# Kernel optimization log

Measured on AMD Instinct MI355X. Metric: run time of the kernel, lower is better.

## Reference

```python
import jax, jax.numpy as jnp
import numpy as np
import math

BATCH, SEQLEN, DMODEL, NSTATE, DFF = 4, 2048, 1024, 16, 4096
EPS = 1e-6


def rmsnorm(x, scale):
    return x * jax.lax.rsqrt(jnp.mean(x * x, axis=-1, keepdims=True) + EPS) * scale


def ssm_scan(u, A_ssm, B_ssm, C_ssm, D_ssm):
    # u: (B, L, D). Diagonal SSM per (d, n) channel/state pair.
    dt = jnp.exp(jnp.linspace(math.log(0.001), math.log(0.1), NSTATE))  # (N,)
    expA = jnp.exp(A_ssm)                 # (D, N); continuous A = -expA
    dA = jnp.exp(-expA * dt)              # (D, N) discrete decay
    dB = B_ssm * (1.0 - dA) / expA        # (D, N) ZOH input matrix

    def step(s, u_t):
        # s: (B, D, N), u_t: (B, D)
        s = s * dA + u_t[..., None] * dB
        y = jnp.einsum('bdn,dn->bd', s, C_ssm)
        return s, y

    s0 = jnp.zeros((u.shape[0], DMODEL, NSTATE), dtype=u.dtype)
    _, ys = jax.lax.scan(step, s0, jnp.transpose(u, (1, 0, 2)))  # ys: (L, B, D)
    return jnp.transpose(ys, (1, 0, 2)) + u * D_ssm


def setup_inputs() -> dict:
    key = jax.random.key(0)
    ks = jax.random.split(key, 6)
    return {
        'x': jax.random.normal(ks[0], (BATCH, SEQLEN, DMODEL), jnp.float32),
        'A_ssm': jax.random.normal(ks[1], (DMODEL, NSTATE), jnp.float32),
        'B_ssm': jax.random.normal(ks[2], (DMODEL, NSTATE), jnp.float32),
        'C_ssm': jax.random.normal(ks[3], (DMODEL, NSTATE), jnp.float32),
        'D_ssm': jnp.zeros((DMODEL,), jnp.float32),
        'scale1': jnp.ones((DMODEL,), jnp.float32),
        'scale2': jnp.ones((DMODEL,), jnp.float32),
        'w1': jax.random.normal(ks[4], (DMODEL, DFF), jnp.float32) * 0.02,
        'b1': jnp.zeros((DFF,), jnp.float32),
        'w2': jax.random.normal(ks[5], (DFF, DMODEL), jnp.float32) * 0.02,
        'b2': jnp.zeros((DMODEL,), jnp.float32),
    }


def reference(x, A_ssm, B_ssm, C_ssm, D_ssm, scale1, scale2, w1, b1, w2, b2):
    x = x + ssm_scan(rmsnorm(x, scale1), A_ssm, B_ssm, C_ssm, D_ssm)
    h = rmsnorm(x, scale2)
    h = jax.nn.gelu(h @ w1 + b1, approximate=False) @ w2 + b2
    return x + h
```

## Files before the change

kernel.cpp:

```cpp
#include <hip/hip_runtime.h>
#include <cstdint>
#include <cstddef>


#define BATCH 4
#define SEQLEN 2048
#define DMODEL 1024
#define NSTATE 16
#define DFF 4096
#define NCH 32
#define LCH 64

typedef unsigned short ushort_t;
typedef __attribute__((ext_vector_type(8))) short short8;
typedef __attribute__((ext_vector_type(4))) float f32x4;

__device__ __forceinline__ ushort_t f2bf(float f) {
  uint32_t u = __builtin_bit_cast(uint32_t, f);
  uint32_t r = (u + 0x7FFFu + ((u >> 16) & 1u)) >> 16;
  return (ushort_t)r;
}

__global__ void coef_kernel(const float* __restrict__ A_ssm, const float* __restrict__ B_ssm,
                            const float* __restrict__ C_ssm,
                            float* __restrict__ dA_t, float* __restrict__ dBz_t,
                            float* __restrict__ dAc_t, float* __restrict__ Ct) {
  int d = blockIdx.x * 256 + threadIdx.x;
  if (d >= DMODEL) return;
  const float l0 = -6.907755278982137f;
  const float ld = 0.30701134573253947f;
  for (int n = 0; n < NSTATE; n++) {
    float dt = expf(l0 + (float)n * ld);
    float a  = A_ssm[d * NSTATE + n];
    float ea = expf(a);
    float da = expf(-ea * dt);
    float dbz = B_ssm[d * NSTATE + n] * (1.f - da) / ea;
    float dac = expf(-ea * dt * (float)LCH);
    dA_t [n * DMODEL + d] = da;
    dBz_t[n * DMODEL + d] = dbz;
    dAc_t[n * DMODEL + d] = dac;
    Ct   [n * DMODEL + d] = C_ssm[d * NSTATE + n];
  }
}

__global__ void transpose_to_bf16(const float* __restrict__ src, ushort_t* __restrict__ dst,
                                  int R, int C) {
  __shared__ float tile[32][33];
  int bx = blockIdx.x * 32, by = blockIdx.y * 32;
  int tx = threadIdx.x, ty = threadIdx.y;
  #pragma unroll
  for (int i = 0; i < 4; i++) {
    int r = by + ty + i * 8;
    tile[ty + i * 8][tx] = src[(size_t)r * C + bx + tx];
  }
  __syncthreads();
  #pragma unroll
  for (int i = 0; i < 4; i++) {
    int c = bx + ty + i * 8;
    dst[(size_t)c * R + by + tx] = f2bf(tile[tx][ty + i * 8]);
  }
}

__global__ void rms1_kernel(const float* __restrict__ x, float* __restrict__ rrms) {
  int row = blockIdx.x * 4 + (threadIdx.x >> 6);
  int lane = threadIdx.x & 63;
  const float4* p = (const float4*)(x + (size_t)row * DMODEL);
  float s = 0.f;
  #pragma unroll
  for (int w = 0; w < 4; w++) {
    float4 v = p[w * 64 + lane];
    s += v.x * v.x + v.y * v.y + v.z * v.z + v.w * v.w;
  }
  #pragma unroll
  for (int off = 32; off; off >>= 1) s += __shfl_xor(s, off, 64);
  if (lane == 0) rrms[row] = rsqrtf(s * (1.f / DMODEL) + 1e-6f);
}

__global__ void scan_pass1(const float* __restrict__ x, const float* __restrict__ rrms,
                           const float* __restrict__ scale1,
                           const float* __restrict__ dA_t, const float* __restrict__ dBz_t,
                           float* __restrict__ s_fin) {
  int d = blockIdx.x * 256 + threadIdx.x;
  int b = blockIdx.y, c = blockIdx.z;
  float dA[NSTATE], dBz[NSTATE], s[NSTATE];
  #pragma unroll
  for (int n = 0; n < NSTATE; n++) {
    dA[n] = dA_t[n * DMODEL + d];
    dBz[n] = dBz_t[n * DMODEL + d];
    s[n] = 0.f;
  }
  float sc1 = scale1[d];
  const float* xp = x + ((size_t)b * SEQLEN + (size_t)c * LCH) * DMODEL + d;
  const float* rp = rrms + b * SEQLEN + c * LCH;
  for (int t = 0; t < LCH; t++) {
    float u = xp[(size_t)t * DMODEL] * rp[t] * sc1;
    #pragma unroll
    for (int n = 0; n < NSTATE; n++) s[n] = fmaf(s[n], dA[n], u * dBz[n]);
  }
  #pragma unroll
  for (int n = 0; n < NSTATE; n++)
    s_fin[(((size_t)n * BATCH + b) * NCH + c) * DMODEL + d] = s[n];
}

__global__ void scan_pass2(const float* __restrict__ s_fin, const float* __restrict__ dAc_t,
                           float* __restrict__ s_in) {
  int idx = blockIdx.x * 256 + threadIdx.x;
  int d = idx & (DMODEL - 1);
  int b = (idx >> 10) & (BATCH - 1);
  int n = idx >> 12;
  float dc = dAc_t[n * DMODEL + d];
  float s = 0.f;
  for (int c = 0; c < NCH; c++) {
    size_t o = (((size_t)n * BATCH + b) * NCH + c) * DMODEL + d;
    s_in[o] = s;
    s = s_fin[o] + dc * s;
  }
}

__global__ void scan_pass3(const float* __restrict__ x, const float* __restrict__ rrms,
                           const float* __restrict__ scale1,
                           const float* __restrict__ dA_t, const float* __restrict__ dBz_t,
                           const float* __restrict__ Ct, const float* __restrict__ Dv,
                           const float* __restrict__ s_in, float* __restrict__ out) {
  int d = blockIdx.x * 256 + threadIdx.x;
  int b = blockIdx.y, c = blockIdx.z;
  float dA[NSTATE], dBz[NSTATE], Cc[NSTATE], s[NSTATE];
  #pragma unroll
  for (int n = 0; n < NSTATE; n++) {
    dA[n] = dA_t[n * DMODEL + d];
    dBz[n] = dBz_t[n * DMODEL + d];
    Cc[n] = Ct[n * DMODEL + d];
    s[n] = s_in[(((size_t)n * BATCH + b) * NCH + c) * DMODEL + d];
  }
  float sc1 = scale1[d], Dd = Dv[d];
  const float* xp = x + ((size_t)b * SEQLEN + (size_t)c * LCH) * DMODEL + d;
  const float* rp = rrms + b * SEQLEN + c * LCH;
  float* op = out + ((size_t)b * SEQLEN + (size_t)c * LCH) * DMODEL + d;
  for (int t = 0; t < LCH; t++) {
    float xv = xp[(size_t)t * DMODEL];
    float u = xv * rp[t] * sc1;
    float y = 0.f;
    #pragma unroll
    for (int n = 0; n < NSTATE; n++) {
      s[n] = fmaf(s[n], dA[n], u * dBz[n]);
      y = fmaf(Cc[n], s[n], y);
    }
    op[(size_t)t * DMODEL] = xv + y + u * Dd;
  }
}

__global__ void rms2_kernel(const float* __restrict__ x2, const float* __restrict__ scale2,
                            ushort_t* __restrict__ hb) {
  int row = blockIdx.x * 4 + (threadIdx.x >> 6);
  int lane = threadIdx.x & 63;
  const float4* p = (const float4*)(x2 + (size_t)row * DMODEL);
  float4 v[4];
  float s = 0.f;
  #pragma unroll
  for (int w = 0; w < 4; w++) {
    v[w] = p[w * 64 + lane];
    s += v[w].x * v[w].x + v[w].y * v[w].y + v[w].z * v[w].z + v[w].w * v[w].w;
  }
  #pragma unroll
  for (int off = 32; off; off >>= 1) s += __shfl_xor(s, off, 64);
  float r = rsqrtf(s * (1.f / DMODEL) + 1e-6f);
  const float4* sc = (const float4*)scale2;
  #pragma unroll
  for (int w = 0; w < 4; w++) {
    float4 scv = sc[w * 64 + lane];
    ushort4 u;
    u.x = f2bf(v[w].x * r * scv.x);
    u.y = f2bf(v[w].y * r * scv.y);
    u.z = f2bf(v[w].z * r * scv.z);
    u.w = f2bf(v[w].w * r * scv.w);
    *(ushort4*)(hb + (size_t)row * DMODEL + (size_t)(w * 64 + lane) * 4) = u;
  }
}

template <int N>
__device__ __forceinline__ void fence_vm() {
  asm volatile("s_waitcnt vmcnt(%0)" :: "n"(N) : "memory");
}

__device__ __forceinline__ void bar() { asm volatile("s_barrier" ::: "memory"); }

__device__ __forceinline__ void gl2lds16(const ushort_t* g, ushort_t* l) {
  __builtin_amdgcn_global_load_lds(
      (const __attribute__((address_space(1))) unsigned int*)g,
      (__attribute__((address_space(3))) unsigned int*)l, 16, 0, 0);
}

template <int K>
__global__ __launch_bounds__(1024, 4) void gemm_w64(const ushort_t* __restrict__ A,
                                                    const ushort_t* __restrict__ B,
                                                    const float* __restrict__ bias,
                                                    ushort_t* __restrict__ outp,
                                                    int M, int N) {
  constexpr int SLOT = 32768;
  constexpr int NT = K / 64;
  __shared__ __align__(16) ushort_t lds[2 * SLOT];

  const int tid = threadIdx.x;
  const int wave = tid >> 6, lane = tid & 63;
  const int wr = wave >> 2, wc = wave & 3;

  const int nwg = gridDim.x, cpx = nwg >> 3, bid = blockIdx.x;
  const int wg = (bid & 7) * cpx + (bid >> 3);
  const int nbn = N / 256;
  const int m0 = (wg / nbn) * 256, n0 = (wg % nbn) * 256;

  const int scol = 8 * ((tid & 7) ^ ((tid >> 3) & 7));
  const int wo = wave * 512;
  const ushort_t* aStg = A + (size_t)(m0 + (tid >> 3)) * K + scol;
  const ushort_t* aStg2 = aStg + (size_t)128 * K;
  const ushort_t* bStg = B + (size_t)(n0 + (tid >> 3)) * K + scol;
  const ushort_t* bStg2 = bStg + (size_t)128 * K;

  f32x4 acc[4][4] = {};

  {
    ushort_t* d = lds + wo;
    gl2lds16(aStg,  d);
    gl2lds16(aStg2, d + 8192);
    gl2lds16(bStg,  d + 16384);
    gl2lds16(bStg2, d + 24576);
    aStg += 64; aStg2 += 64; bStg += 64; bStg2 += 64;
  }
  fence_vm<0>(); bar();

  const int rl = lane & 15, c4 = lane >> 4;
  const int sw0 = (c4 ^ (rl & 7)) * 8;
  const int sw1 = ((4 | c4) ^ (rl & 7)) * 8;
  const int aOff = (wr * 64 + rl) * 64;
  const int bOff = 16384 + (wc * 64 + rl) * 64;

  const ushort_t* rSlot = lds;
  ushort_t*       wSlot = lds + SLOT;

  for (int t = 0; t < NT; ++t) {
    if (t + 1 < NT) {
      gl2lds16(aStg,  wSlot + wo);
      gl2lds16(aStg2, wSlot + 8192 + wo);
      gl2lds16(bStg,  wSlot + 16384 + wo);
      gl2lds16(bStg2, wSlot + 24576 + wo);
      aStg += 64; aStg2 += 64; bStg += 64; bStg2 += 64;
    }

    const ushort_t* ra0 = rSlot + aOff + sw0;
    const ushort_t* ra1 = rSlot + aOff + sw1;
    const ushort_t* rb0 = rSlot + bOff + sw0;
    const ushort_t* rb1 = rSlot + bOff + sw1;

    {
      short8 af[4], bf[4];
      #pragma unroll
      for (int m = 0; m < 4; m++) af[m] = *(const short8*)(ra0 + m * 1024);
      #pragma unroll
      for (int n = 0; n < 4; n++) bf[n] = *(const short8*)(rb0 + n * 1024);
      __builtin_amdgcn_s_setprio(1);
      #pragma unroll
      for (int m = 0; m < 4; m++)
        #pragma unroll
        for (int n = 0; n < 4; n++)
          acc[m][n] = __builtin_amdgcn_mfma_f32_16x16x32_bf16(af[m], bf[n], acc[m][n], 0, 0, 0);
      __builtin_amdgcn_s_setprio(0);
    }
    {
      short8 af[4], bf[4];
      #pragma unroll
      for (int m = 0; m < 4; m++) af[m] = *(const short8*)(ra1 + m * 1024);
      #pragma unroll
      for (int n = 0; n < 4; n++) bf[n] = *(const short8*)(rb1 + n * 1024);
      __builtin_amdgcn_s_setprio(1);
      #pragma unroll
      for (int m = 0; m < 4; m++)
        #pragma unroll
        for (int n = 0; n < 4; n++)
          acc[m][n] = __builtin_amdgcn_mfma_f32_16x16x32_bf16(af[m], bf[n], acc[m][n], 0, 0, 0);
      __builtin_amdgcn_s_setprio(0);
    }

    if (t + 1 < NT) { fence_vm<0>(); bar(); }
    const ushort_t* tmp = rSlot; rSlot = wSlot; wSlot = (ushort_t*)tmp;
  }

  const int colb = n0 + wc * 64 + rl;
  const int rowb = m0 + wr * 64 + c4 * 4;
  #pragma unroll
  for (int n = 0; n < 4; n++) {
    int col = colb + n * 16;
    float bs = bias[col];
    #pragma unroll
    for (int m = 0; m < 4; m++) {
      int row = rowb + m * 16;
      #pragma unroll
      for (int j = 0; j < 4; j++) {
        float v = acc[m][n][j] + bs;
        float g = v / (1.f + __expf(-1.702f * v));
        outp[(size_t)(row + j) * N + col] = f2bf(g);
      }
    }
  }
}

template <int K, int MODE>
__global__ __launch_bounds__(1024, 4) void gemm16v(const ushort_t* __restrict__ A,
                                                   const ushort_t* __restrict__ B,
                                                   const float* __restrict__ bias,
                                                   const float* __restrict__ resid,
                                                   void* __restrict__ outp,
                                                   int M, int N) {
  constexpr int TILEA = 16384;
  constexpr int SLOT  = TILEA + 8192;
  constexpr int NT = K / 64;
  __shared__ __align__(16) ushort_t lds[3 * SLOT];

  const int tid = threadIdx.x;
  const int wave = tid >> 6, lane = tid & 63;
  const int wr = wave >> 2, wc = wave & 3;

  const int nwg = gridDim.x, cpx = nwg >> 3, bid = blockIdx.x;
  const int wg = (bid & 7) * cpx + (bid >> 3);
  const int nbn = N / 128;
  const int m0 = (wg / nbn) * 256, n0 = (wg % nbn) * 128;

  const int scol = 8 * ((tid & 7) ^ ((tid >> 3) & 7));
  const int wo = wave * 512;

  const ushort_t* aStgLo = A + (size_t)(m0 + (tid >> 3)) * K + scol;
  const ushort_t* aStgHi = aStgLo + (size_t)128 * K;
  const ushort_t* bStg   = B + (size_t)(n0 + (tid >> 3)) * K + scol;

  f32x4 acc[4][2] = {};

  {
    ushort_t* s0p = lds;
    gl2lds16(aStgLo, s0p + wo);
    gl2lds16(aStgHi, s0p + 8192 + wo);
    gl2lds16(bStg,   s0p + TILEA + wo);
    ushort_t* s1p = lds + SLOT;
    gl2lds16(aStgLo + 64, s1p + wo);
    gl2lds16(aStgHi + 64, s1p + 8192 + wo);
    gl2lds16(bStg   + 64, s1p + TILEA + wo);
    aStgLo += 128; aStgHi += 128; bStg += 128;
  }
  fence_vm<3>(); bar();

  const int rl = lane & 15, c4 = lane >> 4;
  const int sw0 = (c4 ^ (rl & 7)) * 8;
  const int sw1 = ((4 | c4) ^ (rl & 7)) * 8;
  const int aOff = (wr * 64 + rl) * 64;
  const int bOff = TILEA + (wc * 32 + rl) * 64;

  const ushort_t* rSlot = lds;
  ushort_t*       wSlot = lds + 2 * SLOT;

  for (int t = 0; t < NT; ++t) {
    const ushort_t* ra0 = rSlot + aOff + sw0;
    const ushort_t* ra1 = rSlot + aOff + sw1;
    const ushort_t* rb0 = rSlot + bOff + sw0;
    const ushort_t* rb1 = rSlot + bOff + sw1;

    short8 af[2][4], bf[2][2];
    #pragma unroll
    for (int m = 0; m < 4; m++) {
      af[0][m] = *(const short8*)(ra0 + m * 1024);
      af[1][m] = *(const short8*)(ra1 + m * 1024);
    }
    #pragma unroll
    for (int n = 0; n < 2; n++) {
      bf[0][n] = *(const short8*)(rb0 + n * 1024);
      bf[1][n] = *(const short8*)(rb1 + n * 1024);
    }

    if (t + 2 < NT) {
      gl2lds16(aStgLo, wSlot + wo);
      gl2lds16(aStgHi, wSlot + 8192 + wo);
      gl2lds16(bStg,   wSlot + TILEA + wo);
      aStgLo += 64; aStgHi += 64; bStg += 64;
    }

    __builtin_amdgcn_s_setprio(1);
    #pragma unroll
    for (int kk = 0; kk < 2; kk++)
      #pragma unroll
      for (int m = 0; m < 4; m++)
        #pragma unroll
        for (int n = 0; n < 2; n++)
          acc[m][n] = __builtin_amdgcn_mfma_f32_16x16x32_bf16(af[kk][m], bf[kk][n],
                                                              acc[m][n], 0, 0, 0);
    __builtin_amdgcn_s_setprio(0);

    if (t + 2 < NT) fence_vm<3>();
    else            fence_vm<0>();
    bar();

    const ushort_t* rn = rSlot + SLOT;
    rSlot = (rn == lds + 3 * SLOT) ? lds : rn;
    ushort_t* wn = wSlot + SLOT;
    wSlot = (wn == lds + 3 * SLOT) ? lds : wn;
  }

  const int colb = n0 + wc * 32 + rl;
  const int rowb = m0 + wr * 64 + c4 * 4;
  #pragma unroll
  for (int n = 0; n < 2; n++) {
    int col = colb + n * 16;
    float bs = bias[col];
    #pragma unroll
    for (int m = 0; m < 4; m++) {
      int row = rowb + m * 16;
      #pragma unroll
      for (int j = 0; j < 4; j++) {
        float v = acc[m][n][j] + bs;
        size_t o = (size_t)(row + j) * N + col;
        if (MODE == 1) {
          float g = v / (1.f + __expf(-1.702f * v));
          ((ushort_t*)outp)[o] = f2bf(g);
        } else {
          ((float*)outp)[o] = resid[o] + v;
        }
      }
    }
  }
}

extern "C" void kernel_launch(void* const* d_in, const int* in_sizes, int n_in,
                              void* d_out, int out_size, void* d_ws, size_t ws_size,
                              hipStream_t stream) {
  (void)in_sizes; (void)n_in; (void)out_size; (void)ws_size;
  const float* x      = (const float*)d_in[0];
  const float* A_ssm  = (const float*)d_in[1];
  const float* B_ssm  = (const float*)d_in[2];
  const float* C_ssm  = (const float*)d_in[3];
  const float* D_ssm  = (const float*)d_in[4];
  const float* scale1 = (const float*)d_in[5];
  const float* scale2 = (const float*)d_in[6];
  const float* w1     = (const float*)d_in[7];
  const float* b1     = (const float*)d_in[8];
  const float* w2     = (const float*)d_in[9];
  const float* b2     = (const float*)d_in[10];
  float* out = (float*)d_out;

  char* ws = (char*)d_ws;
  float*    rrms  = (float*)(ws + 0);
  float*    dA_t  = (float*)(ws + 32768);
  float*    dBz_t = (float*)(ws + 98304);
  float*    dAc_t = (float*)(ws + 163840);
  float*    Ct    = (float*)(ws + 229376);
  float*    s_fin = (float*)(ws + 294912);
  float*    s_in  = (float*)(ws + 8683520);
  ushort_t* hb    = (ushort_t*)(ws + 17072128);
  ushort_t* w1t   = (ushort_t*)(ws + 33849344);
  ushort_t* w2t   = (ushort_t*)(ws + 42237952);
  ushort_t* gb    = (ushort_t*)(ws + 50626560);

  const int ROWS = BATCH * SEQLEN;

  coef_kernel<<<DMODEL / 256, 256, 0, stream>>>(A_ssm, B_ssm, C_ssm, dA_t, dBz_t, dAc_t, Ct);
  transpose_to_bf16<<<dim3(DFF / 32, DMODEL / 32), dim3(32, 8), 0, stream>>>(w1, w1t, DMODEL, DFF);
  transpose_to_bf16<<<dim3(DMODEL / 32, DFF / 32), dim3(32, 8), 0, stream>>>(w2, w2t, DFF, DMODEL);
  rms1_kernel<<<ROWS / 4, 256, 0, stream>>>(x, rrms);
  scan_pass1<<<dim3(DMODEL / 256, BATCH, NCH), 256, 0, stream>>>(x, rrms, scale1, dA_t, dBz_t, s_fin);
  scan_pass2<<<(BATCH * DMODEL * NSTATE) / 256, 256, 0, stream>>>(s_fin, dAc_t, s_in);
  scan_pass3<<<dim3(DMODEL / 256, BATCH, NCH), 256, 0, stream>>>(x, rrms, scale1, dA_t, dBz_t, Ct,
                                                                 D_ssm, s_in, out);
  rms2_kernel<<<ROWS / 4, 256, 0, stream>>>(out, scale2, hb);

  gemm_w64<DMODEL><<<(ROWS / 256) * (DFF / 256), 1024, 0, stream>>>(
      hb, w1t, b1, gb, ROWS, DFF);
  gemm16v<DFF, 2><<<(ROWS / 256) * (DMODEL / 128), 1024, 0, stream>>>(
      gb, w2t, b2, out, out, ROWS, DMODEL);
}
```

Before: 211.0 us.

## Shrink first GEMM tile to 256x128 with 8 waves and K-step 32

Replaces the first FFN GEMM kernel with a smaller 256x128 block tile, 512 threads and a K step of 32. The LDS swizzle and staging layout are rebuilt to match. LDS per block drops from 128KB to 48KB, so more blocks can be resident and the grid doubles in size. In exchange, each tile gets less data reuse, and there are twice as many barrier and sync points per K.

```diff
diff --git a/kernel.cpp b/kernel.cpp
--- a/kernel.cpp
+++ b/kernel.cpp
@@ -191,94 +191,69 @@
 }
 
 template <int K>
-__global__ __launch_bounds__(1024, 4) void gemm_w64(const ushort_t* __restrict__ A,
-                                                    const ushort_t* __restrict__ B,
-                                                    const float* __restrict__ bias,
-                                                    ushort_t* __restrict__ outp,
-                                                    int M, int N) {
-  constexpr int SLOT = 32768;
-  constexpr int NT = K / 64;
+__global__ __launch_bounds__(512, 4) void gemm_h64(const ushort_t* __restrict__ A,
+                                                   const ushort_t* __restrict__ B,
+                                                   const float* __restrict__ bias,
+                                                   ushort_t* __restrict__ outp,
+                                                   int M, int N) {
+  constexpr int SLOT = 12288;
+  constexpr int NT = K / 32;
   __shared__ __align__(16) ushort_t lds[2 * SLOT];
 
   const int tid = threadIdx.x;
   const int wave = tid >> 6, lane = tid & 63;
-  const int wr = wave >> 2, wc = wave & 3;
+  const int wr = wave >> 1, wc = wave & 1;
 
   const int nwg = gridDim.x, cpx = nwg >> 3, bid = blockIdx.x;
   const int wg = (bid & 7) * cpx + (bid >> 3);
-  const int nbn = N / 256;
-  const int m0 = (wg / nbn) * 256, n0 = (wg % nbn) * 256;
-
-  const int scol = 8 * ((tid & 7) ^ ((tid >> 3) & 7));
+  const int nbn = N / 128;
+  const int m0 = (wg / nbn) * 256, n0 = (wg % nbn) * 128;
+
+  const int scol = 8 * ((tid & 3) ^ ((tid >> 3) & 3));
   const int wo = wave * 512;
-  const ushort_t* aStg = A + (size_t)(m0 + (tid >> 3)) * K + scol;
-  const ushort_t* aStg2 = aStg + (size_t)128 * K;
-  const ushort_t* bStg = B + (size_t)(n0 + (tid >> 3)) * K + scol;
-  const ushort_t* bStg2 = bStg + (size_t)128 * K;
+  const ushort_t* aStgLo = A + (size_t)(m0 + (tid >> 2)) * K + scol;
+  const ushort_t* aStgHi = aStgLo + (size_t)128 * K;
+  const ushort_t* bStg   = B + (size_t)(n0 + (tid >> 2)) * K + scol;
 
   f32x4 acc[4][4] = {};
 
-  {
-    ushort_t* d = lds + wo;
-    gl2lds16(aStg,  d);
-    gl2lds16(aStg2, d + 8192);
-    gl2lds16(bStg,  d + 16384);
-    gl2lds16(bStg2, d + 24576);
-    aStg += 64; aStg2 += 64; bStg += 64; bStg2 += 64;
-  }
+  gl2lds16(aStgLo, lds + wo);
+  gl2lds16(aStgHi, lds + 4096 + wo);
+  gl2lds16(bStg,   lds + 8192 + wo);
+  aStgLo += 32; aStgHi += 32; bStg += 32;
   fence_vm<0>(); bar();
 
   const int rl = lane & 15, c4 = lane >> 4;
-  const int sw0 = (c4 ^ (rl & 7)) * 8;
-  const int sw1 = ((4 | c4) ^ (rl & 7)) * 8;
-  const int aOff = (wr * 64 + rl) * 64;
-  const int bOff = 16384 + (wc * 64 + rl) * 64;
+  const int cswz = (c4 ^ ((rl >> 1) & 3)) * 8;
+  const int aOff = (wr * 64 + rl) * 32;
+  const int bOff = 8192 + (wc * 64 + rl) * 32;
 
   const ushort_t* rSlot = lds;
   ushort_t*       wSlot = lds + SLOT;
 
   for (int t = 0; t < NT; ++t) {
     if (t + 1 < NT) {
-      gl2lds16(aStg,  wSlot + wo);
-      gl2lds16(aStg2, wSlot + 8192 + wo);
-      gl2lds16(bStg,  wSlot + 16384 + wo);
-      gl2lds16(bStg2, wSlot + 24576 + wo);
-      aStg += 64; aStg2 += 64; bStg += 64; bStg2 += 64;
-    }
-
-    const ushort_t* ra0 = rSlot + aOff + sw0;
-    const ushort_t* ra1 = rSlot + aOff + sw1;
-    const ushort_t* rb0 = rSlot + bOff + sw0;
-    const ushort_t* rb1 = rSlot + bOff + sw1;
-
-    {
-      short8 af[4], bf[4];
+      gl2lds16(aStgLo, wSlot + wo);
+      gl2lds16(aStgHi, wSlot + 4096 + wo);
+      gl2lds16(bStg,   wSlot + 8192 + wo);
+      aStgLo += 32; aStgHi += 32; bStg += 32;
+    }
+
+    const ushort_t* ra = rSlot + aOff + cswz;
+    const ushort_t* rb = rSlot + bOff + cswz;
+    short8 af[4], bf[4];
+    #pragma unroll
+    for (int m = 0; m < 4; m++) af[m] = *(const short8*)(ra + m * 512);
+    #pragma unroll
+    for (int n = 0; n < 4; n++) bf[n] = *(const short8*)(rb + n * 512);
+
+    __builtin_amdgcn_s_setprio(1);
+    #pragma unroll
+    for (int m = 0; m < 4; m++)
       #pragma unroll
-      for (int m = 0; m < 4; m++) af[m] = *(const short8*)(ra0 + m * 1024);
-      #pragma unroll
-      for (int n = 0; n < 4; n++) bf[n] = *(const short8*)(rb0 + n * 1024);
-      __builtin_amdgcn_s_setprio(1);
-      #pragma unroll
-      for (int m = 0; m < 4; m++)
-        #pragma unroll
-        for (int n = 0; n < 4; n++)
-          acc[m][n] = __builtin_amdgcn_mfma_f32_16x16x32_bf16(af[m], bf[n], acc[m][n], 0, 0, 0);
-      __builtin_amdgcn_s_setprio(0);
-    }
-    {
-      short8 af[4], bf[4];
-      #pragma unroll
-      for (int m = 0; m < 4; m++) af[m] = *(const short8*)(ra1 + m * 1024);
-      #pragma unroll
-      for (int n = 0; n < 4; n++) bf[n] = *(const short8*)(rb1 + n * 1024);
-      __builtin_amdgcn_s_setprio(1);
-      #pragma unroll
-      for (int m = 0; m < 4; m++)
-        #pragma unroll
-        for (int n = 0; n < 4; n++)
-          acc[m][n] = __builtin_amdgcn_mfma_f32_16x16x32_bf16(af[m], bf[n], acc[m][n], 0, 0, 0);
-      __builtin_amdgcn_s_setprio(0);
-    }
+      for (int n = 0; n < 4; n++)
+        acc[m][n] = __builtin_amdgcn_mfma_f32_16x16x32_bf16(af[m], bf[n], acc[m][n], 0, 0, 0);
+    __builtin_amdgcn_s_setprio(0);
 
     if (t + 1 < NT) { fence_vm<0>(); bar(); }
     const ushort_t* tmp = rSlot; rSlot = wSlot; wSlot = (ushort_t*)tmp;
@@ -467,7 +442,7 @@
                                                                  D_ssm, s_in, out);
   rms2_kernel<<<ROWS / 4, 256, 0, stream>>>(out, scale2, hb);
 
-  gemm_w64<DMODEL><<<(ROWS / 256) * (DFF / 256), 1024, 0, stream>>>(
+  gemm_h64<DMODEL><<<(ROWS / 256) * (DFF / 128), 512, 0, stream>>>(
       hb, w1t, b1, gb, ROWS, DFF);
   gemm16v<DFF, 2><<<(ROWS / 256) * (DMODEL / 128), 1024, 0, stream>>>(
       gb, w2t, b2, out, out, ROWS, DMODEL);
```

Result: no change. 215.3 us (+2.0%).

## Fuse RMSNorms into scan passes and shorten scan chunks

Applied to the files above, without the earlier changes.

The first RMSNorm is folded into the scan's first pass and into its third pass, using 1024-thread blocks that each cover one 16-row chunk across the full model width. The second RMSNorm and its bf16 conversion are also folded into the third pass, which removes the separate norm kernels and the round trips through global memory. Chunk length drops from 64 to 16, so there are 128 chunks, more blocks, and a longer sequential carry pass. The larger s_fin/s_in buffers now share space with the GEMM intermediate buffer, and the RMS reduction over x is computed twice.

```diff
diff --git a/kernel.cpp b/kernel.cpp
--- a/kernel.cpp
+++ b/kernel.cpp
@@ -8,8 +8,8 @@
 #define DMODEL 1024
 #define NSTATE 16
 #define DFF 4096
-#define NCH 32
-#define LCH 64
+#define NCH 128
+#define LCH 16
 
 typedef unsigned short ushort_t;
 typedef __attribute__((ext_vector_type(8))) short short8;
@@ -61,27 +61,28 @@
   }
 }
 
-__global__ void rms1_kernel(const float* __restrict__ x, float* __restrict__ rrms) {
-  int row = blockIdx.x * 4 + (threadIdx.x >> 6);
-  int lane = threadIdx.x & 63;
-  const float4* p = (const float4*)(x + (size_t)row * DMODEL);
-  float s = 0.f;
-  #pragma unroll
-  for (int w = 0; w < 4; w++) {
-    float4 v = p[w * 64 + lane];
-    s += v.x * v.x + v.y * v.y + v.z * v.z + v.w * v.w;
-  }
-  #pragma unroll
-  for (int off = 32; off; off >>= 1) s += __shfl_xor(s, off, 64);
-  if (lane == 0) rrms[row] = rsqrtf(s * (1.f / DMODEL) + 1e-6f);
-}
-
-__global__ void scan_pass1(const float* __restrict__ x, const float* __restrict__ rrms,
-                           const float* __restrict__ scale1,
-                           const float* __restrict__ dA_t, const float* __restrict__ dBz_t,
-                           float* __restrict__ s_fin) {
-  int d = blockIdx.x * 256 + threadIdx.x;
-  int b = blockIdx.y, c = blockIdx.z;
+__global__ void fused_scan1(const float* __restrict__ x, const float* __restrict__ scale1,
+                            const float* __restrict__ dA_t, const float* __restrict__ dBz_t,
+                            float* __restrict__ s_fin) {
+  const int b = blockIdx.x >> 7, c = blockIdx.x & 127;
+  const int tid = threadIdx.x, wave = tid >> 6, lane = tid & 63;
+  __shared__ float rrmsL[LCH];
+
+  {
+    const float4* p = (const float4*)(x + ((size_t)b * SEQLEN + (size_t)c * LCH + wave) * DMODEL);
+    float s = 0.f;
+    #pragma unroll
+    for (int w = 0; w < 4; w++) {
+      float4 v = p[w * 64 + lane];
+      s += v.x * v.x + v.y * v.y + v.z * v.z + v.w * v.w;
+    }
+    #pragma unroll
+    for (int off = 32; off; off >>= 1) s += __shfl_xor(s, off, 64);
+    if (lane == 0) rrmsL[wave] = rsqrtf(s * (1.f / DMODEL) + 1e-6f);
+  }
+  __syncthreads();
+
+  const int d = tid;
   float dA[NSTATE], dBz[NSTATE], s[NSTATE];
   #pragma unroll
   for (int n = 0; n < NSTATE; n++) {
@@ -89,11 +90,11 @@
     dBz[n] = dBz_t[n * DMODEL + d];
     s[n] = 0.f;
   }
-  float sc1 = scale1[d];
+  const float sc1 = scale1[d];
   const float* xp = x + ((size_t)b * SEQLEN + (size_t)c * LCH) * DMODEL + d;
-  const float* rp = rrms + b * SEQLEN + c * LCH;
+  #pragma unroll
   for (int t = 0; t < LCH; t++) {
-    float u = xp[(size_t)t * DMODEL] * rp[t] * sc1;
+    float u = xp[(size_t)t * DMODEL] * rrmsL[t] * sc1;
     #pragma unroll
     for (int n = 0; n < NSTATE; n++) s[n] = fmaf(s[n], dA[n], u * dBz[n]);
   }
@@ -117,63 +118,83 @@
   }
 }
 
-__global__ void scan_pass3(const float* __restrict__ x, const float* __restrict__ rrms,
-                           const float* __restrict__ scale1,
-                           const float* __restrict__ dA_t, const float* __restrict__ dBz_t,
-                           const float* __restrict__ Ct, const float* __restrict__ Dv,
-                           const float* __restrict__ s_in, float* __restrict__ out) {
-  int d = blockIdx.x * 256 + threadIdx.x;
-  int b = blockIdx.y, c = blockIdx.z;
-  float dA[NSTATE], dBz[NSTATE], Cc[NSTATE], s[NSTATE];
-  #pragma unroll
-  for (int n = 0; n < NSTATE; n++) {
-    dA[n] = dA_t[n * DMODEL + d];
-    dBz[n] = dBz_t[n * DMODEL + d];
-    Cc[n] = Ct[n * DMODEL + d];
-    s[n] = s_in[(((size_t)n * BATCH + b) * NCH + c) * DMODEL + d];
-  }
-  float sc1 = scale1[d], Dd = Dv[d];
-  const float* xp = x + ((size_t)b * SEQLEN + (size_t)c * LCH) * DMODEL + d;
-  const float* rp = rrms + b * SEQLEN + c * LCH;
-  float* op = out + ((size_t)b * SEQLEN + (size_t)c * LCH) * DMODEL + d;
-  for (int t = 0; t < LCH; t++) {
-    float xv = xp[(size_t)t * DMODEL];
-    float u = xv * rp[t] * sc1;
-    float y = 0.f;
+__global__ void fused_scan3(const float* __restrict__ x, const float* __restrict__ scale1,
+                            const float* __restrict__ scale2,
+                            const float* __restrict__ dA_t, const float* __restrict__ dBz_t,
+                            const float* __restrict__ Ct, const float* __restrict__ Dv,
+                            const float* __restrict__ s_in,
+                            float* __restrict__ out, ushort_t* __restrict__ hb) {
+  const int b = blockIdx.x >> 7, c = blockIdx.x & 127;
+  const int tid = threadIdx.x, wave = tid >> 6, lane = tid & 63;
+  const size_t rowBase = (size_t)b * SEQLEN + (size_t)c * LCH;
+  __shared__ float rrmsL[LCH];
+
+  {
+    const float4* p = (const float4*)(x + (rowBase + wave) * DMODEL);
+    float s = 0.f;
+    #pragma unroll
+    for (int w = 0; w < 4; w++) {
+      float4 v = p[w * 64 + lane];
+      s += v.x * v.x + v.y * v.y + v.z * v.z + v.w * v.w;
+    }
+    #pragma unroll
+    for (int off = 32; off; off >>= 1) s += __shfl_xor(s, off, 64);
+    if (lane == 0) rrmsL[wave] = rsqrtf(s * (1.f / DMODEL) + 1e-6f);
+  }
+  __syncthreads();
+
+  {
+    const int d = tid;
+    float dA[NSTATE], dBz[NSTATE], Cc[NSTATE], s[NSTATE];
     #pragma unroll
     for (int n = 0; n < NSTATE; n++) {
-      s[n] = fmaf(s[n], dA[n], u * dBz[n]);
-      y = fmaf(Cc[n], s[n], y);
-    }
-    op[(size_t)t * DMODEL] = xv + y + u * Dd;
-  }
-}
-
-__global__ void rms2_kernel(const float* __restrict__ x2, const float* __restrict__ scale2,
-                            ushort_t* __restrict__ hb) {
-  int row = blockIdx.x * 4 + (threadIdx.x >> 6);
-  int lane = threadIdx.x & 63;
-  const float4* p = (const float4*)(x2 + (size_t)row * DMODEL);
-  float4 v[4];
-  float s = 0.f;
-  #pragma unroll
-  for (int w = 0; w < 4; w++) {
-    v[w] = p[w * 64 + lane];
-    s += v[w].x * v[w].x + v[w].y * v[w].y + v[w].z * v[w].z + v[w].w * v[w].w;
-  }
-  #pragma unroll
-  for (int off = 32; off; off >>= 1) s += __shfl_xor(s, off, 64);
-  float r = rsqrtf(s * (1.f / DMODEL) + 1e-6f);
-  const float4* sc = (const float4*)scale2;
-  #pragma unroll
-  for (int w = 0; w < 4; w++) {
-    float4 scv = sc[w * 64 + lane];
-    ushort4 u;
-    u.x = f2bf(v[w].x * r * scv.x);
-    u.y = f2bf(v[w].y * r * scv.y);
-    u.z = f2bf(v[w].z * r * scv.z);
-    u.w = f2bf(v[w].w * r * scv.w);
-    *(ushort4*)(hb + (size_t)row * DMODEL + (size_t)(w * 64 + lane) * 4) = u;
+      dA[n] = dA_t[n * DMODEL + d];
+      dBz[n] = dBz_t[n * DMODEL + d];
+      Cc[n] = Ct[n * DMODEL + d];
+      s[n] = s_in[(((size_t)n * BATCH + b) * NCH + c) * DMODEL + d];
+    }
+    const float sc1 = scale1[d], Dd = Dv[d];
+    const float* xp = x + rowBase * DMODEL + d;
+    float* op = out + rowBase * DMODEL + d;
+    #pragma unroll
+    for (int t = 0; t < LCH; t++) {
+      float xv = xp[(size_t)t * DMODEL];
+      float u = xv * rrmsL[t] * sc1;
+      float y = 0.f;
+      #pragma unroll
+      for (int n = 0; n < NSTATE; n++) {
+        s[n] = fmaf(s[n], dA[n], u * dBz[n]);
+        y = fmaf(Cc[n], s[n], y);
+      }
+      op[(size_t)t * DMODEL] = xv + y + u * Dd;
+    }
+  }
+  __syncthreads();
+
+  {
+    const float4* p = (const float4*)(out + (rowBase + wave) * DMODEL);
+    float4 v[4];
+    float s = 0.f;
+    #pragma unroll
+    for (int w = 0; w < 4; w++) {
+      v[w] = p[w * 64 + lane];
+      s += v[w].x * v[w].x + v[w].y * v[w].y + v[w].z * v[w].z + v[w].w * v[w].w;
+    }
+    #pragma unroll
+    for (int off = 32; off; off >>= 1) s += __shfl_xor(s, off, 64);
+    float r = rsqrtf(s * (1.f / DMODEL) + 1e-6f);
+    const float4* sc = (const float4*)scale2;
+    ushort_t* hrow = hb + (rowBase + wave) * DMODEL;
+    #pragma unroll
+    for (int w = 0; w < 4; w++) {
+      float4 scv = sc[w * 64 + lane];
+      ushort4 u;
+      u.x = f2bf(v[w].x * r * scv.x);
+      u.y = f2bf(v[w].y * r * scv.y);
+      u.z = f2bf(v[w].z * r * scv.z);
+      u.w = f2bf(v[w].w * r * scv.w);
+      *(ushort4*)(hrow + (size_t)(w * 64 + lane) * 4) = u;
+    }
   }
 }
 
@@ -443,29 +464,26 @@
   float* out = (float*)d_out;
 
   char* ws = (char*)d_ws;
-  float*    rrms  = (float*)(ws + 0);
   float*    dA_t  = (float*)(ws + 32768);
   float*    dBz_t = (float*)(ws + 98304);
   float*    dAc_t = (float*)(ws + 163840);
   float*    Ct    = (float*)(ws + 229376);
-  float*    s_fin = (float*)(ws + 294912);
-  float*    s_in  = (float*)(ws + 8683520);
   ushort_t* hb    = (ushort_t*)(ws + 17072128);
   ushort_t* w1t   = (ushort_t*)(ws + 33849344);
   ushort_t* w2t   = (ushort_t*)(ws + 42237952);
   ushort_t* gb    = (ushort_t*)(ws + 50626560);
+  float*    s_fin = (float*)(ws + 50626560);
+  float*    s_in  = (float*)(ws + 50626560 + 33554432);
 
   const int ROWS = BATCH * SEQLEN;
 
   coef_kernel<<<DMODEL / 256, 256, 0, stream>>>(A_ssm, B_ssm, C_ssm, dA_t, dBz_t, dAc_t, Ct);
   transpose_to_bf16<<<dim3(DFF / 32, DMODEL / 32), dim3(32, 8), 0, stream>>>(w1, w1t, DMODEL, DFF);
   transpose_to_bf16<<<dim3(DMODEL / 32, DFF / 32), dim3(32, 8), 0, stream>>>(w2, w2t, DFF, DMODEL);
-  rms1_kernel<<<ROWS / 4, 256, 0, stream>>>(x, rrms);
-  scan_pass1<<<dim3(DMODEL / 256, BATCH, NCH), 256, 0, stream>>>(x, rrms, scale1, dA_t, dBz_t, s_fin);
+  fused_scan1<<<BATCH * NCH, 1024, 0, stream>>>(x, scale1, dA_t, dBz_t, s_fin);
   scan_pass2<<<(BATCH * DMODEL * NSTATE) / 256, 256, 0, stream>>>(s_fin, dAc_t, s_in);
-  scan_pass3<<<dim3(DMODEL / 256, BATCH, NCH), 256, 0, stream>>>(x, rrms, scale1, dA_t, dBz_t, Ct,
-                                                                 D_ssm, s_in, out);
-  rms2_kernel<<<ROWS / 4, 256, 0, stream>>>(out, scale2, hb);
+  fused_scan3<<<BATCH * NCH, 1024, 0, stream>>>(x, scale1, scale2, dA_t, dBz_t, Ct,
+                                                D_ssm, s_in, out, hb);
 
   gemm_w64<DMODEL><<<(ROWS / 256) * (DFF / 256), 1024, 0, stream>>>(
       hb, w1t, b1, gb, ROWS, DFF);
```

After: 222.8 us. +5.5%, slower.

## Replace second GEMM with 128x128 tile, double-buffered kernel for more workgroups

Applied to the files above, without the earlier changes.

The down-projection GEMM now uses a 128x128 output tile instead of 256x128, which doubles the number of workgroups to 512 and gives better CU coverage. It also switches from a 3-slot LDS pipeline with prefetch depth 2 to a 2-slot double buffer with a full drain each iteration. Smaller tiles reduce per-workgroup LDS and registers and raise occupancy. The cost is lower arithmetic intensity and more global traffic, and the shallower pipeline may expose more memory latency.

```diff
diff --git a/kernel.cpp b/kernel.cpp
--- a/kernel.cpp
+++ b/kernel.cpp
@@ -303,17 +303,16 @@
   }
 }
 
-template <int K, int MODE>
-__global__ __launch_bounds__(1024, 4) void gemm16v(const ushort_t* __restrict__ A,
-                                                   const ushort_t* __restrict__ B,
-                                                   const float* __restrict__ bias,
-                                                   const float* __restrict__ resid,
-                                                   void* __restrict__ outp,
-                                                   int M, int N) {
-  constexpr int TILEA = 16384;
-  constexpr int SLOT  = TILEA + 8192;
+template <int K>
+__global__ __launch_bounds__(1024, 8) void gemm2_128(const ushort_t* __restrict__ A,
+                                                     const ushort_t* __restrict__ B,
+                                                     const float* __restrict__ bias,
+                                                     const float* __restrict__ resid,
+                                                     float* __restrict__ outp,
+                                                     int M, int N) {
+  constexpr int SLOT = 16384;
   constexpr int NT = K / 64;
-  __shared__ __align__(16) ushort_t lds[3 * SLOT];
+  __shared__ __align__(16) ushort_t lds[2 * SLOT];
 
   const int tid = threadIdx.x;
   const int wave = tid >> 6, lane = tid & 63;
@@ -322,104 +321,82 @@
   const int nwg = gridDim.x, cpx = nwg >> 3, bid = blockIdx.x;
   const int wg = (bid & 7) * cpx + (bid >> 3);
   const int nbn = N / 128;
-  const int m0 = (wg / nbn) * 256, n0 = (wg % nbn) * 128;
+  const int m0 = (wg / nbn) * 128, n0 = (wg % nbn) * 128;
 
   const int scol = 8 * ((tid & 7) ^ ((tid >> 3) & 7));
   const int wo = wave * 512;
-
-  const ushort_t* aStgLo = A + (size_t)(m0 + (tid >> 3)) * K + scol;
-  const ushort_t* aStgHi = aStgLo + (size_t)128 * K;
-  const ushort_t* bStg   = B + (size_t)(n0 + (tid >> 3)) * K + scol;
-
-  f32x4 acc[4][2] = {};
-
-  {
-    ushort_t* s0p = lds;
-    gl2lds16(aStgLo, s0p + wo);
-    gl2lds16(aStgHi, s0p + 8192 + wo);
-    gl2lds16(bStg,   s0p + TILEA + wo);
-    ushort_t* s1p = lds + SLOT;
-    gl2lds16(aStgLo + 64, s1p + wo);
-    gl2lds16(aStgHi + 64, s1p + 8192 + wo);
-    gl2lds16(bStg   + 64, s1p + TILEA + wo);
-    aStgLo += 128; aStgHi += 128; bStg += 128;
-  }
-  fence_vm<3>(); bar();
+  const ushort_t* aStg = A + (size_t)(m0 + (tid >> 3)) * K + scol;
+  const ushort_t* bStg = B + (size_t)(n0 + (tid >> 3)) * K + scol;
+
+  f32x4 acc[2][2] = {};
+
+  gl2lds16(aStg, lds + wo);
+  gl2lds16(bStg, lds + 8192 + wo);
+  aStg += 64; bStg += 64;
+  fence_vm<0>(); bar();
 
   const int rl = lane & 15, c4 = lane >> 4;
   const int sw0 = (c4 ^ (rl & 7)) * 8;
   const int sw1 = ((4 | c4) ^ (rl & 7)) * 8;
-  const int aOff = (wr * 64 + rl) * 64;
-  const int bOff = TILEA + (wc * 32 + rl) * 64;
+  const int aOff = (wr * 32 + rl) * 64;
+  const int bOff = 8192 + (wc * 32 + rl) * 64;
 
   const ushort_t* rSlot = lds;
-  ushort_t*       wSlot = lds + 2 * SLOT;
+  ushort_t*       wSlot = lds + SLOT;
 
   for (int t = 0; t < NT; ++t) {
-    const ushort_t* ra0 = rSlot + aOff + sw0;
-    const ushort_t* ra1 = rSlot + aOff + sw1;
-    const ushort_t* rb0 = rSlot + bOff + sw0;
-    const ushort_t* rb1 = rSlot + bOff + sw1;
-
-    short8 af[2][4], bf[2][2];
-    #pragma unroll
-    for (int m = 0; m < 4; m++) {
-      af[0][m] = *(const short8*)(ra0 + m * 1024);
-      af[1][m] = *(const short8*)(ra1 + m * 1024);
-    }
-    #pragma unroll
-    for (int n = 0; n < 2; n++) {
-      bf[0][n] = *(const short8*)(rb0 + n * 1024);
-      bf[1][n] = *(const short8*)(rb1 + n * 1024);
-    }
-
-    if (t + 2 < NT) {
-      gl2lds16(aStgLo, wSlot + wo);
-      gl2lds16(aStgHi, wSlot + 8192 + wo);
-      gl2lds16(bStg,   wSlot + TILEA + wo);
-      aStgLo += 64; aStgHi += 64; bStg += 64;
-    }
-
-    __builtin_amdgcn_s_setprio(1);
-    #pragma unroll
-    for (int kk = 0; kk < 2; kk++)
-      #pragma unroll
-      for (int m = 0; m < 4; m++)
+    if (t + 1 < NT) {
+      gl2lds16(aStg, wSlot + wo);
+      gl2lds16(bStg, wSlot + 8192 + wo);
+      aStg += 64; bStg += 64;
+    }
+
+    {
+      short8 af[2], bf[2];
+      af[0] = *(const short8*)(rSlot + aOff + sw0);
+      af[1] = *(const short8*)(rSlot + aOff + sw0 + 1024);
+      bf[0] = *(const short8*)(rSlot + bOff + sw0);
+      bf[1] = *(const short8*)(rSlot + bOff + sw0 + 1024);
+      __builtin_amdgcn_s_setprio(1);
+      #pragma unroll
+      for (int m = 0; m < 2; m++)
         #pragma unroll
         for (int n = 0; n < 2; n++)
-          acc[m][n] = __builtin_amdgcn_mfma_f32_16x16x32_bf16(af[kk][m], bf[kk][n],
-                                                              acc[m][n], 0, 0, 0);
-    __builtin_amdgcn_s_setprio(0);
-
-    if (t + 2 < NT) fence_vm<3>();
-    else            fence_vm<0>();
-    bar();
-
-    const ushort_t* rn = rSlot + SLOT;
-    rSlot = (rn == lds + 3 * SLOT) ? lds : rn;
-    ushort_t* wn = wSlot + SLOT;
-    wSlot = (wn == lds + 3 * SLOT) ? lds : wn;
+          acc[m][n] = __builtin_amdgcn_mfma_f32_16x16x32_bf16(af[m], bf[n], acc[m][n], 0, 0, 0);
+      __builtin_amdgcn_s_setprio(0);
+    }
+    {
+      short8 af[2], bf[2];
+      af[0] = *(const short8*)(rSlot + aOff + sw1);
+      af[1] = *(const short8*)(rSlot + aOff + sw1 + 1024);
+      bf[0] = *(const short8*)(rSlot + bOff + sw1);
+      bf[1] = *(const short8*)(rSlot + bOff + sw1 + 1024);
+      __builtin_amdgcn_s_setprio(1);
+      #pragma unroll
+      for (int m = 0; m < 2; m++)
+        #pragma unroll
+        for (int n = 0; n < 2; n++)
+          acc[m][n] = __builtin_amdgcn_mfma_f32_16x16x32_bf16(af[m], bf[n], acc[m][n], 0, 0, 0);
+      __builtin_amdgcn_s_setprio(0);
+    }
+
+    if (t + 1 < NT) { fence_vm<0>(); bar(); }
+    const ushort_t* tmp = rSlot; rSlot = wSlot; wSlot = (ushort_t*)tmp;
   }
 
   const int colb = n0 + wc * 32 + rl;
-  const int rowb = m0 + wr * 64 + c4 * 4;
+  const int rowb = m0 + wr * 32 + c4 * 4;
   #pragma unroll
   for (int n = 0; n < 2; n++) {
     int col = colb + n * 16;
     float bs = bias[col];
     #pragma unroll
-    for (int m = 0; m < 4; m++) {
+    for (int m = 0; m < 2; m++) {
       int row = rowb + m * 16;
       #pragma unroll
       for (int j = 0; j < 4; j++) {
-        float v = acc[m][n][j] + bs;
         size_t o = (size_t)(row + j) * N + col;
-        if (MODE == 1) {
-          float g = v / (1.f + __expf(-1.702f * v));
-          ((ushort_t*)outp)[o] = f2bf(g);
-        } else {
-          ((float*)outp)[o] = resid[o] + v;
-        }
+        outp[o] = resid[o] + acc[m][n][j] + bs;
       }
     }
   }
@@ -469,6 +446,6 @@
 
   gemm_w64<DMODEL><<<(ROWS / 256) * (DFF / 256), 1024, 0, stream>>>(
       hb, w1t, b1, gb, ROWS, DFF);
-  gemm16v<DFF, 2><<<(ROWS / 256) * (DMODEL / 128), 1024, 0, stream>>>(
+  gemm2_128<DFF><<<(ROWS / 128) * (DMODEL / 128), 1024, 0, stream>>>(
       gb, w2t, b2, out, out, ROWS, DMODEL);
 }
```

Result: no change. 214.6 us (+1.7%).
